# Optimization experiments

Hardware: AMD Instinct MI355X
Metric: run time of the kernel (lower is better)

Reference implementation:

```python
import jax, jax.numpy as jnp
import numpy as np
from jax import lax

B, T, F, H, V, L = 64, 80, 4096, 512, 32000, 31


def _rn(k, shape, scale=0.05):
    return jax.random.normal(k, shape, dtype=jnp.float32) * scale


def setup_inputs() -> dict:
    key = jax.random.key(0)
    ks = jax.random.split(key, 16)
    emb = _rn(ks[0], (V, H)).at[0].set(0.0)  # padding_idx=0 row zeroed
    return dict(
        video_features=jax.random.normal(ks[1], (B, T, F), jnp.float32),
        captions=jax.random.randint(ks[2], (B, L), 0, V, jnp.int64),
        emb=emb,
        enc_Wih=_rn(ks[3], (4 * H, F)), enc_Whh=_rn(ks[4], (4 * H, H)),
        enc_bih=_rn(ks[5], (4 * H,)), enc_bhh=_rn(ks[6], (4 * H,)),
        attn_W=_rn(ks[7], (H, 2 * H)), attn_b=_rn(ks[8], (H,)),
        v_w=_rn(ks[9], (H,)),
        dec_Wih=_rn(ks[10], (4 * H, 2 * H)), dec_Whh=_rn(ks[11], (4 * H, H)),
        dec_bih=_rn(ks[12], (4 * H,)), dec_bhh=_rn(ks[13], (4 * H,)),
        fc_W=_rn(ks[14], (V, H)), fc_b=_rn(ks[15], (V,)),
    )


def _lstm_step(x, h, c, Wih, Whh, bih, bhh):
    # PyTorch gate order: i, f, g, o
    g = x @ Wih.T + bih + h @ Whh.T + bhh
    i, f, gg, o = jnp.split(g, 4, axis=-1)
    c = jax.nn.sigmoid(f) * c + jax.nn.sigmoid(i) * jnp.tanh(gg)
    h = jax.nn.sigmoid(o) * jnp.tanh(c)
    return h, c


def reference(video_features, captions, emb, enc_Wih, enc_Whh, enc_bih, enc_bhh,
              attn_W, attn_b, v_w, dec_Wih, dec_Whh, dec_bih, dec_bhh, fc_W, fc_b):
    b = video_features.shape[0]
    h_dim = enc_Whh.shape[1]
    h0 = jnp.zeros((b, h_dim), video_features.dtype)
    c0 = jnp.zeros((b, h_dim), video_features.dtype)

    # ---- encoder LSTM over time ----
    def enc_step(carry, x):
        h, c = carry
        h, c = _lstm_step(x, h, c, enc_Wih, enc_Whh, enc_bih, enc_bhh)
        return (h, c), h

    (h, c), enc_out = lax.scan(enc_step, (h0, c0), video_features.transpose(1, 0, 2))
    enc_out = enc_out.transpose(1, 0, 2)  # [B, T, H]

    # ---- attentive decoder, teacher forcing always on ----
    tokens = captions[:, :-1].T  # [L-1, B]

    def dec_step(carry, tok):
        h, c = carry
        e = emb[tok]  # [B, H]
        # Bahdanau attention: v . tanh(W [h; enc_out])
        hrep = jnp.broadcast_to(h[:, None, :], enc_out.shape)
        energy = jnp.tanh(jnp.concatenate([hrep, enc_out], axis=2) @ attn_W.T + attn_b)
        scores = energy @ v_w  # [B, T]
        w = jax.nn.softmax(scores, axis=1)
        ctx = jnp.einsum('bt,bth->bh', w, enc_out)
        x = jnp.concatenate([e, ctx], axis=1)  # [B, 2H]
        h, c = _lstm_step(x, h, c, dec_Wih, dec_Whh, dec_bih, dec_bhh)
        logits = h @ fc_W.T + fc_b  # [B, V]
        return (h, c), logits

    _, outs = lax.scan(dec_step, (h, c), tokens)
    return outs.transpose(1, 0, 2)  # [B, L-1, V]
```

## Files before the change

### kernel.cpp

```cpp
#include <hip/hip_runtime.h>


#define DEV __device__ __forceinline__

typedef __attribute__((ext_vector_type(4))) float f32x4;
typedef __attribute__((ext_vector_type(8))) short bf16x8;
typedef _Float16 half2_t __attribute__((ext_vector_type(2)));

static constexpr int B_ = 64, T_ = 80, H_ = 512, L_ = 31, NDEC = 30;

DEV unsigned short f2bf(float f) {
  unsigned u = __builtin_bit_cast(unsigned, f);
  u += 0x7FFF + ((u >> 16) & 1);
  return (unsigned short)(u >> 16);
}
DEV float bf2f(unsigned short s) {
  unsigned u = (unsigned)s << 16;
  return __builtin_bit_cast(float, u);
}
DEV unsigned short f2h(float x) { return __builtin_bit_cast(unsigned short, (_Float16)x); }
DEV float h2f(unsigned short h) { return (float)__builtin_bit_cast(_Float16, h); }
DEV unsigned f2h2(float lo, float hi) { return (unsigned)f2h(lo) | ((unsigned)f2h(hi) << 16); }
DEV float fdot2(unsigned x, unsigned w, float acc) {
  return __builtin_amdgcn_fdot2(__builtin_bit_cast(half2_t, x),
                                __builtin_bit_cast(half2_t, w), acc, false);
}
DEV float4 acc8(float4 a, uint4 hv, uint4 w0, uint4 w1, uint4 w2, uint4 w3) {
  a.x = fdot2(hv.x, w0.x, a.x); a.y = fdot2(hv.x, w0.y, a.y);
  a.z = fdot2(hv.x, w0.z, a.z); a.w = fdot2(hv.x, w0.w, a.w);
  a.x = fdot2(hv.y, w1.x, a.x); a.y = fdot2(hv.y, w1.y, a.y);
  a.z = fdot2(hv.y, w1.z, a.z); a.w = fdot2(hv.y, w1.w, a.w);
  a.x = fdot2(hv.z, w2.x, a.x); a.y = fdot2(hv.z, w2.y, a.y);
  a.z = fdot2(hv.z, w2.z, a.z); a.w = fdot2(hv.z, w2.w, a.w);
  a.x = fdot2(hv.w, w3.x, a.x); a.y = fdot2(hv.w, w3.y, a.y);
  a.z = fdot2(hv.w, w3.z, a.z); a.w = fdot2(hv.w, w3.w, a.w);
  return a;
}
DEV float accS(float s, uint4 hv, uint4 w) {
  s = fdot2(hv.x, w.x, s); s = fdot2(hv.y, w.y, s);
  s = fdot2(hv.z, w.z, s); s = fdot2(hv.w, w.w, s);
  return s;
}
DEV float sigmoidf(float x) { return 1.f / (1.f + __expf(-x)); }
DEV float tanh_fast(float x) { float e = __expf(2.f * x); return (e - 1.f) / (e + 1.f); }

DEV void astf(float* p, float v) { __hip_atomic_store(p, v, __ATOMIC_RELAXED, __HIP_MEMORY_SCOPE_AGENT); }
DEV void astu(unsigned* p, unsigned v) { __hip_atomic_store(p, v, __ATOMIC_RELAXED, __HIP_MEMORY_SCOPE_AGENT); }
DEV void asti(int* p, int v) { __hip_atomic_store(p, v, __ATOMIC_RELAXED, __HIP_MEMORY_SCOPE_AGENT); }
DEV float aldf(const float* p) { return __hip_atomic_load((float*)p, __ATOMIC_RELAXED, __HIP_MEMORY_SCOPE_AGENT); }
DEV unsigned aldu(const unsigned* p) { return __hip_atomic_load((unsigned*)p, __ATOMIC_RELAXED, __HIP_MEMORY_SCOPE_AGENT); }
DEV int aldi(const int* p) { return __hip_atomic_load((int*)p, __ATOMIC_RELAXED, __HIP_MEMORY_SCOPE_AGENT); }

DEV void tsync(int* tf, int m, int ph) {
  __syncthreads();
  if (threadIdx.x == 0) asti(tf + m * 16, ph);
  if (threadIdx.x < 4)
    while (aldi(tf + (int)threadIdx.x * 16) < ph) __builtin_amdgcn_s_sleep(1);
  __syncthreads();
}

__global__ __launch_bounds__(256) void k_cvt(const float* __restrict__ in,
                                             unsigned short* __restrict__ out, long n4) {
  long i = (long)blockIdx.x * 256 + threadIdx.x;
  long stride = (long)gridDim.x * 256;
  for (; i < n4; i += stride) {
    float4 v = reinterpret_cast<const float4*>(in)[i];
    ushort4 o;
    o.x = f2bf(v.x); o.y = f2bf(v.y); o.z = f2bf(v.z); o.w = f2bf(v.w);
    reinterpret_cast<ushort4*>(out)[i] = o;
  }
}

__global__ void k_detect_i64(const int* __restrict__ cap, int* __restrict__ flag) {
  __shared__ int s;
  if (threadIdx.x == 0) s = 0;
  __syncthreads();
  int acc = 0;
  for (int i = threadIdx.x; i < (B_ * L_) / 2; i += 256) acc |= cap[2 * i + 1];
  if (acc) atomicOr(&s, 1);
  __syncthreads();
  if (threadIdx.x == 0) flag[0] = (s == 0) ? 1 : 0;
}

__global__ __launch_bounds__(256) void k_gather_emb(const float* __restrict__ emb,
                                                    const int* __restrict__ cap,
                                                    const int* __restrict__ flag,
                                                    unsigned short* __restrict__ aemb) {
  int r = blockIdx.x;
  int l = r >> 6, b = r & 63;
  int ci = b * L_ + l;
  int tok = flag[0] ? cap[2 * ci] : cap[ci];
  const float* src = emb + (size_t)tok * H_;
  unsigned short* dst = aemb + (size_t)r * H_;
  for (int c = threadIdx.x; c < H_; c += 256) dst[c] = f2bf(src[c]);
}

__global__ __launch_bounds__(256) void k_pack_enc(const float* __restrict__ whh,
                                                  uint4* __restrict__ wpe) {
  int idx = blockIdx.x * 256 + threadIdx.x;
  int k2 = idx >> 9, j = idx & 511;
  float2 r0 = *(const float2*)(whh + (size_t)(j) * 512 + 2 * k2);
  float2 r1 = *(const float2*)(whh + (size_t)(512 + j) * 512 + 2 * k2);
  float2 r2 = *(const float2*)(whh + (size_t)(1024 + j) * 512 + 2 * k2);
  float2 r3 = *(const float2*)(whh + (size_t)(1536 + j) * 512 + 2 * k2);
  wpe[idx] = make_uint4(f2h2(r0.x, r0.y), f2h2(r1.x, r1.y), f2h2(r2.x, r2.y), f2h2(r3.x, r3.y));
}

__global__ __launch_bounds__(256) void k_pack_dec(const float* __restrict__ dwih,
                                                  const float* __restrict__ dwhh,
                                                  uint4* __restrict__ wpd) {
  int idx = blockIdx.x * 256 + threadIdx.x;
  int k2 = idx >> 9, j = idx & 511;
  float2 r[4];
  if (k2 < 256) {
#pragma unroll
    for (int g = 0; g < 4; ++g)
      r[g] = *(const float2*)(dwih + (size_t)(g * 512 + j) * 1024 + 512 + 2 * k2);
  } else {
#pragma unroll
    for (int g = 0; g < 4; ++g)
      r[g] = *(const float2*)(dwhh + (size_t)(g * 512 + j) * 512 + 2 * (k2 - 256));
  }
  wpd[idx] = make_uint4(f2h2(r[0].x, r[0].y), f2h2(r[1].x, r[1].y),
                        f2h2(r[2].x, r[2].y), f2h2(r[3].x, r[3].y));
}

__global__ __launch_bounds__(256) void k_pack_attn2(const float* __restrict__ attnw,
                                                    uint4* __restrict__ wat2) {
  int idx = blockIdx.x * 256 + threadIdx.x;
  int k8 = idx >> 9, u = idx & 511;
  const float* p = attnw + (size_t)u * 1024 + 8 * k8;
  wat2[idx] = make_uint4(f2h2(p[0], p[1]), f2h2(p[2], p[3]),
                         f2h2(p[4], p[5]), f2h2(p[6], p[7]));
}

template <int OUT_MODE>
__global__ __launch_bounds__(256) void k_gemm(const unsigned short* __restrict__ A, int lda,
                                              const unsigned short* __restrict__ Bm, int ldb,
                                              float* __restrict__ C, int N, int K,
                                              const float* __restrict__ bias0,
                                              const float* __restrict__ bias1) {
  __shared__ __align__(16) unsigned short As[128 * 40];
  __shared__ __align__(16) unsigned short Bs[128 * 40];
  const int tid = threadIdx.x;
  const int m0 = blockIdx.y * 128, n0 = blockIdx.x * 128;
  const int wave = tid >> 6, lane = tid & 63;
  const int wm = wave >> 1, wn = wave & 1;
  const int lr = lane & 15, lk = lane >> 4;

  f32x4 acc[4][4];
#pragma unroll
  for (int m = 0; m < 4; ++m)
#pragma unroll
    for (int n = 0; n < 4; ++n) acc[m][n] = (f32x4){0.f, 0.f, 0.f, 0.f};

  const int c0 = tid, c1 = tid + 256;
  const int ar0 = c0 >> 2, as0 = c0 & 3;
  const int ar1 = c1 >> 2, as1 = c1 & 3;
  const unsigned short* pa0 = A + (size_t)(m0 + ar0) * lda + as0 * 8;
  const unsigned short* pa1 = A + (size_t)(m0 + ar1) * lda + as1 * 8;
  const unsigned short* pb0 = Bm + (size_t)(n0 + ar0) * ldb + as0 * 8;
  const unsigned short* pb1 = Bm + (size_t)(n0 + ar1) * ldb + as1 * 8;

  uint4 va0 = *(const uint4*)(pa0);
  uint4 va1 = *(const uint4*)(pa1);
  uint4 vb0 = *(const uint4*)(pb0);
  uint4 vb1 = *(const uint4*)(pb1);

  for (int k0 = 0; k0 < K; k0 += 32) {
    *(uint4*)(As + ar0 * 40 + as0 * 8) = va0;
    *(uint4*)(As + ar1 * 40 + as1 * 8) = va1;
    *(uint4*)(Bs + ar0 * 40 + as0 * 8) = vb0;
    *(uint4*)(Bs + ar1 * 40 + as1 * 8) = vb1;
    __syncthreads();
    if (k0 + 32 < K) {
      va0 = *(const uint4*)(pa0 + k0 + 32);
      va1 = *(const uint4*)(pa1 + k0 + 32);
      vb0 = *(const uint4*)(pb0 + k0 + 32);
      vb1 = *(const uint4*)(pb1 + k0 + 32);
    }
    bf16x8 af[4], bfr[4];
#pragma unroll
    for (int m = 0; m < 4; ++m)
      af[m] = *(const bf16x8*)(As + (wm * 64 + m * 16 + lr) * 40 + lk * 8);
#pragma unroll
    for (int n = 0; n < 4; ++n)
      bfr[n] = *(const bf16x8*)(Bs + (wn * 64 + n * 16 + lr) * 40 + lk * 8);
#pragma unroll
    for (int m = 0; m < 4; ++m)
#pragma unroll
      for (int n = 0; n < 4; ++n)
        acc[m][n] = __builtin_amdgcn_mfma_f32_16x16x32_bf16(af[m], bfr[n], acc[m][n], 0, 0, 0);
    __syncthreads();
  }
#pragma unroll
  for (int m = 0; m < 4; ++m) {
#pragma unroll
    for (int n = 0; n < 4; ++n) {
      const int col = n0 + wn * 64 + n * 16 + lr;
      float bv = (bias0 ? bias0[col] : 0.f) + (bias1 ? bias1[col] : 0.f);
#pragma unroll
      for (int j = 0; j < 4; ++j) {
        const int row = m0 + wm * 64 + m * 16 + lk * 4 + j;
        float v = acc[m][n][j] + bv;
        if (OUT_MODE == 0) {
          C[(size_t)row * N + col] = v;
        } else if (OUT_MODE == 1) {
          int l = row >> 6, b = row & 63;
          C[((size_t)b * NDEC + l) * (size_t)N + col] = v;
        } else {
          C[((size_t)row * 512 + (col & 511)) * 4 + (col >> 9)] = v;
        }
      }
    }
  }
}

__global__ __launch_bounds__(1024) void k_enc4(const float4* __restrict__ xg4,
                                               const uint4* __restrict__ wpe,
                                               float* __restrict__ encf,
                                               unsigned short* __restrict__ encbf,
                                               float* __restrict__ cfin,
                                               unsigned* __restrict__ h16E,
                                               int* __restrict__ flagsE) {
  __shared__ __align__(16) unsigned short h16[512];
  __shared__ __align__(16) float psum[8 * 4 * 128];
  __shared__ unsigned short hnew[128];
  const int bid = blockIdx.x, b = bid >> 2, m = bid & 3, tid = threadIdx.x;
  const int j128 = tid & 127, ks = tid >> 7;
  const int j = m * 128 + j128;
  int* tf = flagsE + b * 64;
  float c = 0.f;
  if (tid < 256) ((unsigned*)h16)[tid] = 0u;
  __syncthreads();
  const uint4* hp4 = (const uint4*)h16;
  for (int t = 0; t < T_; ++t) {
    float4 a = {0.f, 0.f, 0.f, 0.f}, a1 = a;
#pragma unroll 2
    for (int k8 = ks * 8; k8 < ks * 8 + 8; k8 += 2) {
      uint4 h0 = hp4[k8], h1 = hp4[k8 + 1];
      a = acc8(a, h0, wpe[((k8 * 4 + 0) << 9) | j], wpe[((k8 * 4 + 1) << 9) | j],
               wpe[((k8 * 4 + 2) << 9) | j], wpe[((k8 * 4 + 3) << 9) | j]);
      a1 = acc8(a1, h1, wpe[((k8 * 4 + 4) << 9) | j], wpe[((k8 * 4 + 5) << 9) | j],
                wpe[((k8 * 4 + 6) << 9) | j], wpe[((k8 * 4 + 7) << 9) | j]);
    }
    psum[ks * 512 + 0 * 128 + j128] = a.x + a1.x;
    psum[ks * 512 + 1 * 128 + j128] = a.y + a1.y;
    psum[ks * 512 + 2 * 128 + j128] = a.z + a1.z;
    psum[ks * 512 + 3 * 128 + j128] = a.w + a1.w;
    __syncthreads();
    if (tid < 128) {
      float4 xa = xg4[((size_t)b * T_ + t) * 512 + m * 128 + tid];
      float g0 = xa.x, g1 = xa.y, g2 = xa.z, g3 = xa.w;
#pragma unroll
      for (int q = 0; q < 8; ++q) {
        g0 += psum[q * 512 + 0 * 128 + tid];
        g1 += psum[q * 512 + 1 * 128 + tid];
        g2 += psum[q * 512 + 2 * 128 + tid];
        g3 += psum[q * 512 + 3 * 128 + tid];
      }
      c = sigmoidf(g1) * c + sigmoidf(g0) * tanh_fast(g2);
      float h = sigmoidf(g3) * tanh_fast(c);
      size_t o = ((size_t)b * T_ + t) * 512 + m * 128 + tid;
      encf[o] = h;
      encbf[o] = f2bf(h);
      hnew[tid] = f2h(h);
      if (t == T_ - 1) cfin[b * 512 + m * 128 + tid] = c;
    }
    __syncthreads();
    const int p = t & 1;
    if (tid < 64)
      astu(h16E + (size_t)p * 64 * 256 + b * 256 + m * 64 + tid,
           (unsigned)hnew[2 * tid] | ((unsigned)hnew[2 * tid + 1] << 16));
    tsync(tf, m, t + 1);
    if (t < T_ - 1) {
      if (tid < 256)
        ((unsigned*)h16)[tid] = aldu(h16E + (size_t)p * 64 * 256 + b * 256 + tid);
      __syncthreads();
    }
  }
}

__global__ __launch_bounds__(1024) void k_dec6(const uint4* __restrict__ wpd,
                                               const uint4* __restrict__ wat2,
                                               const float* __restrict__ vw,
                                               const float4* __restrict__ eg4,
                                               const float* __restrict__ encpart,
                                               const unsigned short* __restrict__ encbf,
                                               const float* __restrict__ encf,
                                               const float* __restrict__ cfin,
                                               unsigned short* __restrict__ hsbf,
                                               float* __restrict__ scpart,
                                               unsigned* __restrict__ ctxpH,
                                               unsigned* __restrict__ h16D,
                                               int* __restrict__ flagsD) {
  __shared__ __align__(16) unsigned short xv16[1024];
  __shared__ float vsm[512];
  __shared__ float hwOwn[128];
  __shared__ float sc[80], wts[80];
  __shared__ __align__(16) float psum1[8 * 128];
  __shared__ __align__(16) float psum[8 * 4 * 128];
  __shared__ __align__(16) float4 ctxp[8 * 128];
  __shared__ unsigned short hnew[128];
  const int bid = blockIdx.x, b = bid >> 2, m = bid & 3, tid = threadIdx.x;
  int* tf = flagsD + b * 64;
  if (tid < 512) {
    vsm[tid] = vw[tid];
    xv16[512 + tid] = f2h(encf[((size_t)b * T_ + T_ - 1) * 512 + tid]);
  }
  float c = 0.f;
  if (tid < 128) c = cfin[b * 512 + m * 128 + tid];
  __syncthreads();
  const uint4* xp4 = (const uint4*)xv16;
  const uint4* xh4 = xp4 + 64;

  for (int l = 0; l < NDEC; ++l) {
    {
      const int u128 = tid & 127, ks = tid >> 7;
      const int u = m * 128 + u128;
      float s = 0.f, s1 = 0.f;
#pragma unroll 2
      for (int k8 = ks * 8; k8 < ks * 8 + 8; k8 += 2) {
        s = accS(s, xh4[k8], wat2[(k8 << 9) | u]);
        s1 = accS(s1, xh4[k8 + 1], wat2[((k8 + 1) << 9) | u]);
      }
      psum1[ks * 128 + u128] = s + s1;
    }
    __syncthreads();
    if (tid < 128) {
      float s = 0.f;
#pragma unroll
      for (int q = 0; q < 8; ++q) s += psum1[q * 128 + tid];
      hwOwn[tid] = s;
    }
    __syncthreads();
    {
      const int wv = tid >> 6, ln = tid & 63;
      for (int t = wv; t < T_; t += 16) {
        const float* ep = encpart + ((size_t)b * T_ + t) * 512 + m * 128;
        float p = vsm[m * 128 + ln] * tanh_fast(hwOwn[ln] + ep[ln]) +
                  vsm[m * 128 + 64 + ln] * tanh_fast(hwOwn[64 + ln] + ep[64 + ln]);
#pragma unroll
        for (int s = 1; s < 64; s <<= 1) p += __shfl_xor(p, s, 64);
        if (ln == 0) astf(scpart + ((size_t)b * 4 + m) * 80 + t, p);
      }
    }
    tsync(tf, m, 3 * l + 1);
    if (tid < 80) {
      float s = 0.f;
#pragma unroll
      for (int mm = 0; mm < 4; ++mm) s += aldf(scpart + ((size_t)b * 4 + mm) * 80 + tid);
      sc[tid] = s;
    }
    __syncthreads();
    if (tid < 64) {
      float x0 = sc[tid];
      float x1 = (tid < 16) ? sc[64 + tid] : -1e30f;
      float mx = fmaxf(x0, x1);
#pragma unroll
      for (int s = 1; s < 64; s <<= 1) mx = fmaxf(mx, __shfl_xor(mx, s, 64));
      float e0 = __expf(x0 - mx);
      float e1 = (tid < 16) ? __expf(x1 - mx) : 0.f;
      float sm = e0 + e1;
#pragma unroll
      for (int s = 1; s < 64; s <<= 1) sm += __shfl_xor(sm, s, 64);
      wts[tid] = e0 / sm;
      if (tid < 16) wts[64 + tid] = e1 / sm;
    }
    __syncthreads();
    {
      const int tsub = tid >> 7, j4 = tid & 127;
      float4 acc = {0.f, 0.f, 0.f, 0.f};
      for (int tl = tsub; tl < 20; tl += 8) {
        const int t = m * 20 + tl;
        float w = wts[t];
        ushort4 e = *(const ushort4*)(encbf + ((size_t)b * T_ + t) * 512 + j4 * 4);
        acc.x += w * bf2f(e.x); acc.y += w * bf2f(e.y);
        acc.z += w * bf2f(e.z); acc.w += w * bf2f(e.w);
      }
      ctxp[tsub * 128 + j4] = acc;
    }
    __syncthreads();
    if (tid < 256) {
      const float* cp = (const float*)ctxp;
      float s0 = 0.f, s1 = 0.f;
#pragma unroll
      for (int q = 0; q < 8; ++q) {
        s0 += cp[q * 512 + 2 * tid];
        s1 += cp[q * 512 + 2 * tid + 1];
      }
      astu(ctxpH + ((size_t)b * 4 + m) * 256 + tid, f2h2(s0, s1));
    }
    tsync(tf, m, 3 * l + 2);
    if (tid < 256) {
      float s0 = 0.f, s1 = 0.f;
#pragma unroll
      for (int mm = 0; mm < 4; ++mm) {
        unsigned u = aldu(ctxpH + ((size_t)b * 4 + mm) * 256 + tid);
        s0 += h2f((unsigned short)(u & 0xffffu));
        s1 += h2f((unsigned short)(u >> 16));
      }
      ((unsigned*)xv16)[tid] = f2h2(s0, s1);
    }
    __syncthreads();
    {
      const int j128 = tid & 127, ks = tid >> 7;
      const int j = m * 128 + j128;
      float4 a = {0.f, 0.f, 0.f, 0.f}, a1 = a;
#pragma unroll 2
      for (int k8 = ks * 16; k8 < ks * 16 + 16; k8 += 2) {
        uint4 h0 = xp4[k8], h1 = xp4[k8 + 1];
        a = acc8(a, h0, wpd[((k8 * 4 + 0) << 9) | j], wpd[((k8 * 4 + 1) << 9) | j],
                 wpd[((k8 * 4 + 2) << 9) | j], wpd[((k8 * 4 + 3) << 9) | j]);
        a1 = acc8(a1, h1, wpd[((k8 * 4 + 4) << 9) | j], wpd[((k8 * 4 + 5) << 9) | j],
                  wpd[((k8 * 4 + 6) << 9) | j], wpd[((k8 * 4 + 7) << 9) | j]);
      }
      psum[ks * 512 + 0 * 128 + j128] = a.x + a1.x;
      psum[ks * 512 + 1 * 128 + j128] = a.y + a1.y;
      psum[ks * 512 + 2 * 128 + j128] = a.z + a1.z;
      psum[ks * 512 + 3 * 128 + j128] = a.w + a1.w;
    }
    __syncthreads();
    if (tid < 128) {
      float4 xa = eg4[((size_t)l * 64 + b) * 512 + m * 128 + tid];
      float g0 = xa.x, g1 = xa.y, g2 = xa.z, g3 = xa.w;
#pragma unroll
      for (int q = 0; q < 8; ++q) {
        g0 += psum[q * 512 + 0 * 128 + tid];
        g1 += psum[q * 512 + 1 * 128 + tid];
        g2 += psum[q * 512 + 2 * 128 + tid];
        g3 += psum[q * 512 + 3 * 128 + tid];
      }
      c = sigmoidf(g1) * c + sigmoidf(g0) * tanh_fast(g2);
      float h = sigmoidf(g3) * tanh_fast(c);
      hsbf[((size_t)l * 64 + b) * 512 + m * 128 + tid] = f2bf(h);
      hnew[tid] = f2h(h);
    }
    __syncthreads();
    const int p = l & 1;
    if (tid < 64)
      astu(h16D + (size_t)p * 64 * 256 + b * 256 + m * 64 + tid,
           (unsigned)hnew[2 * tid] | ((unsigned)hnew[2 * tid + 1] << 16));
    tsync(tf, m, 3 * l + 3);
    if (l < NDEC - 1) {
      if (tid < 256)
        ((unsigned*)xv16)[256 + tid] = aldu(h16D + (size_t)p * 64 * 256 + b * 256 + tid);
      __syncthreads();
    }
  }
}

extern "C" void kernel_launch(void* const* d_in, const int* in_sizes, int n_in,
                              void* d_out, int out_size, void* d_ws, size_t ws_size,
                              hipStream_t stream) {
  const float* video = (const float*)d_in[0];
  const int* captions = (const int*)d_in[1];
  const float* emb = (const float*)d_in[2];
  const float* eWih = (const float*)d_in[3];
  const float* eWhh = (const float*)d_in[4];
  const float* ebih = (const float*)d_in[5];
  const float* ebhh = (const float*)d_in[6];
  const float* attnW = (const float*)d_in[7];
  const float* attnb = (const float*)d_in[8];
  const float* vw = (const float*)d_in[9];
  const float* dWih = (const float*)d_in[10];
  const float* dWhh = (const float*)d_in[11];
  const float* dbih = (const float*)d_in[12];
  const float* dbhh = (const float*)d_in[13];
  const float* fcW = (const float*)d_in[14];
  const float* fcb = (const float*)d_in[15];

  char* ws = (char*)d_ws;
  unsigned short* vid_bf = (unsigned short*)(ws + 0);
  unsigned short* fcw_bf = (unsigned short*)(ws + 0);
  const size_t G = 32768000ull;
  unsigned* h16E = (unsigned*)(ws + G + 0);
  unsigned* h16D = (unsigned*)(ws + G + 131072);
  float* scpartD = (float*)(ws + G + 262144);
  unsigned* ctxpH = (unsigned*)(ws + G + 344064);
  int* flagsE = (int*)(ws + G + 675840);
  int* flagsD = (int*)(ws + G + 692224);
  unsigned short* hs_bf = (unsigned short*)(ws + 33554432ull);
  uint4* wpd = (uint4*)(ws + 35520512ull);
  uint4* wpe = (uint4*)(ws + 39714816ull);
  float* xg4 = (float*)(ws + 41943040ull);
  float* encpart = (float*)(ws + 41943040ull);
  float* eg4 = (float*)(ws + 52428800ull);
  unsigned short* aemb = (unsigned short*)(ws + 68157440ull);
  unsigned short* ewih_bf = (unsigned short*)(ws + 83886080ull);
  float* encf = (float*)(ws + 100663296ull);
  unsigned short* encbf = (unsigned short*)(ws + 111149056ull);
  unsigned short* attnw_bf = (unsigned short*)(ws + 116391936ull);
  unsigned short* dwih_bf = (unsigned short*)(ws + 117440512ull);
  uint4* wat2 = (uint4*)(ws + 121634816ull);
  float* cfin = (float*)(ws + 122159104ull);
  int* flag = (int*)(ws + 122290176ull);

  auto cvt = [&](const float* in, unsigned short* out, long n) {
    long n4 = n / 4;
    int blocks = (int)((n4 + 255) / 256);
    if (blocks > 2048) blocks = 2048;
    k_cvt<<<blocks, 256, 0, stream>>>(in, out, n4);
  };
  cvt(video, vid_bf, 5120L * 4096);
  cvt(eWih, ewih_bf, 2048L * 4096);
  cvt(attnW, attnw_bf, 512L * 1024);
  cvt(dWih, dwih_bf, 2048L * 1024);
  k_detect_i64<<<1, 256, 0, stream>>>(captions, flag);

  k_gemm<2><<<dim3(16, 40), 256, 0, stream>>>(vid_bf, 4096, ewih_bf, 4096, xg4, 2048, 4096, ebih, ebhh);
  cvt(fcW, fcw_bf, 32000L * 512);

  k_pack_enc<<<512, 256, 0, stream>>>(eWhh, wpe);
  k_pack_dec<<<1024, 256, 0, stream>>>(dWih, dWhh, wpd);
  k_pack_attn2<<<128, 256, 0, stream>>>(attnW, wat2);

  hipMemsetAsync(ws + G + 675840, 0, 32768, stream);

  k_enc4<<<256, 1024, 0, stream>>>((const float4*)xg4, wpe, encf, encbf, cfin, h16E, flagsE);

  k_gather_emb<<<1920, 256, 0, stream>>>(emb, captions, flag, aemb);
  k_gemm<0><<<dim3(4, 40), 256, 0, stream>>>(encbf, 512, attnw_bf + 512, 1024, encpart, 512, 512, attnb, nullptr);
  k_gemm<2><<<dim3(16, 15), 256, 0, stream>>>(aemb, 512, dwih_bf, 1024, eg4, 2048, 512, dbih, dbhh);

  k_dec6<<<256, 1024, 0, stream>>>(wpd, wat2, vw, (const float4*)eg4, encpart, encbf, encf,
                                   cfin, hs_bf, scpartD, ctxpH, h16D, flagsD);

  k_gemm<1><<<dim3(250, 15), 256, 0, stream>>>(hs_bf, 512, fcw_bf, 512, (float*)d_out, 32000, 512, fcb, nullptr);
}
```

Before: 1.399 ms.

## Cache encoder recurrent weights in LDS; hoist decoder h-gate matvec before attention

The encoder kernel now loads a quarter of its packed recurrent weight slice (128 KB) into shared memory once. Two of the eight k-slices then read weights from LDS instead of global/L2 on every timestep. The decoder kernel moves the h-dependent half of the LSTM gate matvec into the same phase as the attention query projection, so only the context half remains after the attention syncs. The hoisted partial sums are added to psum later. This shortens the serial critical path between cross-block syncs, but the large LDS allocation may limit occupancy and adds register pressure.

```diff
diff --git a/kernel.cpp b/kernel.cpp
--- a/kernel.cpp
+++ b/kernel.cpp
@@ -216,7 +216,7 @@
   }
 }
 
-__global__ __launch_bounds__(1024) void k_enc4(const float4* __restrict__ xg4,
+__global__ __launch_bounds__(1024) void k_enc5(const float4* __restrict__ xg4,
                                                const uint4* __restrict__ wpe,
                                                float* __restrict__ encf,
                                                unsigned short* __restrict__ encbf,
@@ -226,23 +226,39 @@
   __shared__ __align__(16) unsigned short h16[512];
   __shared__ __align__(16) float psum[8 * 4 * 128];
   __shared__ unsigned short hnew[128];
+  __shared__ __align__(16) uint4 wcache[64 * 128];
   const int bid = blockIdx.x, b = bid >> 2, m = bid & 3, tid = threadIdx.x;
   const int j128 = tid & 127, ks = tid >> 7;
   const int j = m * 128 + j128;
   int* tf = flagsE + b * 64;
   float c = 0.f;
+  for (int i = tid; i < 64 * 128; i += 1024) {
+    int k2 = i >> 7, jj = i & 127;
+    wcache[i] = wpe[(k2 << 9) | (m * 128 + jj)];
+  }
   if (tid < 256) ((unsigned*)h16)[tid] = 0u;
   __syncthreads();
   const uint4* hp4 = (const uint4*)h16;
   for (int t = 0; t < T_; ++t) {
     float4 a = {0.f, 0.f, 0.f, 0.f}, a1 = a;
+    if (ks < 2) {
 #pragma unroll 2
-    for (int k8 = ks * 8; k8 < ks * 8 + 8; k8 += 2) {
-      uint4 h0 = hp4[k8], h1 = hp4[k8 + 1];
-      a = acc8(a, h0, wpe[((k8 * 4 + 0) << 9) | j], wpe[((k8 * 4 + 1) << 9) | j],
-               wpe[((k8 * 4 + 2) << 9) | j], wpe[((k8 * 4 + 3) << 9) | j]);
-      a1 = acc8(a1, h1, wpe[((k8 * 4 + 4) << 9) | j], wpe[((k8 * 4 + 5) << 9) | j],
-                wpe[((k8 * 4 + 6) << 9) | j], wpe[((k8 * 4 + 7) << 9) | j]);
+      for (int k8 = ks * 8; k8 < ks * 8 + 8; k8 += 2) {
+        uint4 h0 = hp4[k8], h1 = hp4[k8 + 1];
+        a = acc8(a, h0, wcache[((k8 * 4 + 0) << 7) | j128], wcache[((k8 * 4 + 1) << 7) | j128],
+                 wcache[((k8 * 4 + 2) << 7) | j128], wcache[((k8 * 4 + 3) << 7) | j128]);
+        a1 = acc8(a1, h1, wcache[((k8 * 4 + 4) << 7) | j128], wcache[((k8 * 4 + 5) << 7) | j128],
+                  wcache[((k8 * 4 + 6) << 7) | j128], wcache[((k8 * 4 + 7) << 7) | j128]);
+      }
+    } else {
+#pragma unroll 2
+      for (int k8 = ks * 8; k8 < ks * 8 + 8; k8 += 2) {
+        uint4 h0 = hp4[k8], h1 = hp4[k8 + 1];
+        a = acc8(a, h0, wpe[((k8 * 4 + 0) << 9) | j], wpe[((k8 * 4 + 1) << 9) | j],
+                 wpe[((k8 * 4 + 2) << 9) | j], wpe[((k8 * 4 + 3) << 9) | j]);
+        a1 = acc8(a1, h1, wpe[((k8 * 4 + 4) << 9) | j], wpe[((k8 * 4 + 5) << 9) | j],
+                  wpe[((k8 * 4 + 6) << 9) | j], wpe[((k8 * 4 + 7) << 9) | j]);
+      }
     }
     psum[ks * 512 + 0 * 128 + j128] = a.x + a1.x;
     psum[ks * 512 + 1 * 128 + j128] = a.y + a1.y;
@@ -281,7 +297,7 @@
   }
 }
 
-__global__ __launch_bounds__(1024) void k_dec6(const uint4* __restrict__ wpd,
+__global__ __launch_bounds__(1024) void k_dec7(const uint4* __restrict__ wpd,
                                                const uint4* __restrict__ wat2,
                                                const float* __restrict__ vw,
                                                const float4* __restrict__ eg4,
@@ -316,15 +332,27 @@
 
   for (int l = 0; l < NDEC; ++l) {
     {
-      const int u128 = tid & 127, ks = tid >> 7;
-      const int u = m * 128 + u128;
-      float s = 0.f, s1 = 0.f;
+      const int j128 = tid & 127, ks = tid >> 7;
+      const int j = m * 128 + j128;
+      float4 aH = {0.f, 0.f, 0.f, 0.f}, aH1 = aH;
+      float sW = 0.f, sW1 = 0.f;
 #pragma unroll 2
-      for (int k8 = ks * 8; k8 < ks * 8 + 8; k8 += 2) {
-        s = accS(s, xh4[k8], wat2[(k8 << 9) | u]);
-        s1 = accS(s1, xh4[k8 + 1], wat2[((k8 + 1) << 9) | u]);
-      }
-      psum1[ks * 128 + u128] = s + s1;
+      for (int i = 0; i < 8; i += 2) {
+        const int kg = 64 + ks * 8 + i;
+        const int ka = ks * 8 + i;
+        uint4 hg0 = xp4[kg], hg1 = xp4[kg + 1];
+        aH = acc8(aH, hg0, wpd[((kg * 4 + 0) << 9) | j], wpd[((kg * 4 + 1) << 9) | j],
+                  wpd[((kg * 4 + 2) << 9) | j], wpd[((kg * 4 + 3) << 9) | j]);
+        aH1 = acc8(aH1, hg1, wpd[((kg * 4 + 4) << 9) | j], wpd[((kg * 4 + 5) << 9) | j],
+                   wpd[((kg * 4 + 6) << 9) | j], wpd[((kg * 4 + 7) << 9) | j]);
+        sW = accS(sW, xh4[ka], wat2[(ka << 9) | j]);
+        sW1 = accS(sW1, xh4[ka + 1], wat2[((ka + 1) << 9) | j]);
+      }
+      psum[ks * 512 + 0 * 128 + j128] = aH.x + aH1.x;
+      psum[ks * 512 + 1 * 128 + j128] = aH.y + aH1.y;
+      psum[ks * 512 + 2 * 128 + j128] = aH.z + aH1.z;
+      psum[ks * 512 + 3 * 128 + j128] = aH.w + aH1.w;
+      psum1[ks * 128 + j128] = sW + sW1;
     }
     __syncthreads();
     if (tid < 128) {
@@ -406,19 +434,20 @@
     {
       const int j128 = tid & 127, ks = tid >> 7;
       const int j = m * 128 + j128;
-      float4 a = {0.f, 0.f, 0.f, 0.f}, a1 = a;
+      float4 aC = {0.f, 0.f, 0.f, 0.f}, aC1 = aC;
 #pragma unroll 2
-      for (int k8 = ks * 16; k8 < ks * 16 + 16; k8 += 2) {
-        uint4 h0 = xp4[k8], h1 = xp4[k8 + 1];
-        a = acc8(a, h0, wpd[((k8 * 4 + 0) << 9) | j], wpd[((k8 * 4 + 1) << 9) | j],
-                 wpd[((k8 * 4 + 2) << 9) | j], wpd[((k8 * 4 + 3) << 9) | j]);
-        a1 = acc8(a1, h1, wpd[((k8 * 4 + 4) << 9) | j], wpd[((k8 * 4 + 5) << 9) | j],
-                  wpd[((k8 * 4 + 6) << 9) | j], wpd[((k8 * 4 + 7) << 9) | j]);
-      }
-      psum[ks * 512 + 0 * 128 + j128] = a.x + a1.x;
-      psum[ks * 512 + 1 * 128 + j128] = a.y + a1.y;
-      psum[ks * 512 + 2 * 128 + j128] = a.z + a1.z;
-      psum[ks * 512 + 3 * 128 + j128] = a.w + a1.w;
+      for (int i = 0; i < 8; i += 2) {
+        const int kc = ks * 8 + i;
+        uint4 h0 = xp4[kc], h1 = xp4[kc + 1];
+        aC = acc8(aC, h0, wpd[((kc * 4 + 0) << 9) | j], wpd[((kc * 4 + 1) << 9) | j],
+                  wpd[((kc * 4 + 2) << 9) | j], wpd[((kc * 4 + 3) << 9) | j]);
+        aC1 = acc8(aC1, h1, wpd[((kc * 4 + 4) << 9) | j], wpd[((kc * 4 + 5) << 9) | j],
+                   wpd[((kc * 4 + 6) << 9) | j], wpd[((kc * 4 + 7) << 9) | j]);
+      }
+      psum[ks * 512 + 0 * 128 + j128] += aC.x + aC1.x;
+      psum[ks * 512 + 1 * 128 + j128] += aC.y + aC1.y;
+      psum[ks * 512 + 2 * 128 + j128] += aC.z + aC1.z;
+      psum[ks * 512 + 3 * 128 + j128] += aC.w + aC1.w;
     }
     __syncthreads();
     if (tid < 128) {
@@ -517,13 +546,13 @@
 
   hipMemsetAsync(ws + G + 675840, 0, 32768, stream);
 
-  k_enc4<<<256, 1024, 0, stream>>>((const float4*)xg4, wpe, encf, encbf, cfin, h16E, flagsE);
+  k_enc5<<<256, 1024, 0, stream>>>((const float4*)xg4, wpe, encf, encbf, cfin, h16E, flagsE);
 
   k_gather_emb<<<1920, 256, 0, stream>>>(emb, captions, flag, aemb);
   k_gemm<0><<<dim3(4, 40), 256, 0, stream>>>(encbf, 512, attnw_bf + 512, 1024, encpart, 512, 512, attnb, nullptr);
   k_gemm<2><<<dim3(16, 15), 256, 0, stream>>>(aemb, 512, dwih_bf, 1024, eg4, 2048, 512, dbih, dbhh);
 
-  k_dec6<<<256, 1024, 0, stream>>>(wpd, wat2, vw, (const float4*)eg4, encpart, encbf, encf,
+  k_dec7<<<256, 1024, 0, stream>>>(wpd, wat2, vw, (const float4*)eg4, encpart, encbf, encf,
                                    cfin, hs_bf, scpartD, ctxpH, h16D, flagsD);
 
   k_gemm<1><<<dim3(250, 15), 256, 0, stream>>>(hs_bf, 512, fcw_bf, 512, (float*)d_out, 32000, 512, fcb, nullptr);
```

Result: faster. 1.334 ms (-4.7%).
